# Optimization experiments

Hardware: AMD Instinct MI355X
Metric: run time of the kernel (lower is better)

## Reference

```python
import jax, jax.numpy as jnp
import numpy as np

NUM_EMBEDDINGS = 1024
EMBEDDING_DIM = 256
COMMITMENT_COST = 0.25


def setup_inputs() -> dict:
    key = jax.random.key(0)
    k1, k2 = jax.random.split(key)
    z = jax.random.normal(k1, (32, 256, 32, 32), dtype=jnp.float32)
    # matches torch init: uniform(-1/K, 1/K)
    codebook = jax.random.uniform(
        k2, (NUM_EMBEDDINGS, EMBEDDING_DIM), dtype=jnp.float32,
        minval=-1.0 / NUM_EMBEDDINGS, maxval=1.0 / NUM_EMBEDDINGS)
    return {"z": z, "codebook": codebook}


def reference(z, codebook):
    B, C, H, W = z.shape
    # b c h w -> (b h w) c
    z_nhwc = jnp.transpose(z, (0, 2, 3, 1))
    zf = z_nhwc.reshape(-1, C)  # [N, D]
    # squared euclidean distances [N, K]
    d = (jnp.sum(zf * zf, axis=1, keepdims=True)
         + jnp.sum(codebook * codebook, axis=1)
         - 2.0 * zf @ codebook.T)
    indices = jnp.argmin(d, axis=1)  # [N]
    zq_nhwc = codebook[indices].reshape(B, H, W, C)
    z_q = jnp.transpose(zq_nhwc, (0, 3, 1, 2))  # [B, C, H, W]

    codebook_loss = jnp.mean((jax.lax.stop_gradient(z_q) - z) ** 2)
    commitment_loss = jnp.mean((z_q - jax.lax.stop_gradient(z)) ** 2)
    vq_loss = codebook_loss + COMMITMENT_COST * commitment_loss

    # straight-through estimator
    z_q_st = z + jax.lax.stop_gradient(z_q - z)
    indices_bhw = indices.reshape(B, H, W)
    return z_q_st, vq_loss, indices_bhw
```

## Files before the change

kernel.cpp:

```cpp
#include <hip/hip_runtime.h>

#define NUM_EMB 1024
#define EMB_DIM 256
#define BATCH   32
#define HW      1024
#define Z_ELEMS (BATCH*EMB_DIM*HW)
#define LOSS_OFF Z_ELEMS
#define IDX_OFF (Z_ELEMS+1)

#define WS_CNORM_OFF 16
#define WS_ZNORM_OFF 2048
#define WS_PACKED_BYTE_OFF 262144
#define WS_NEEDED (WS_PACKED_BYTE_OFF + 32768*8)

typedef float v2f __attribute__((ext_vector_type(2)));

__global__ __launch_bounds__(256) void k_prep(const float* __restrict__ z,
                                              const float* __restrict__ cb,
                                              float* __restrict__ ws,
                                              unsigned long long* __restrict__ packed) {
    int gid = blockIdx.x * 256 + threadIdx.x;
    if (gid == 0) { ws[0] = 0.0f; ((unsigned int*)ws)[1] = 0u; }
    if (blockIdx.x < 4) {
        int k = gid;
        const float* row = cb + (size_t)k * EMB_DIM;
        float half[2];
#pragma unroll
        for (int h = 0; h < 2; ++h) {
            const float* a = row + h * 128;
            float r[8];
#pragma unroll
            for (int j = 0; j < 8; ++j) r[j] = __fmul_rn(a[j], a[j]);
            for (int i = 8; i < 128; i += 8)
#pragma unroll
                for (int j = 0; j < 8; ++j)
                    r[j] = __fadd_rn(r[j], __fmul_rn(a[i + j], a[i + j]));
            half[h] = __fadd_rn(__fadd_rn(__fadd_rn(r[0], r[1]), __fadd_rn(r[2], r[3])),
                                __fadd_rn(__fadd_rn(r[4], r[5]), __fadd_rn(r[6], r[7])));
        }
        ws[WS_CNORM_OFF + k] = __fadd_rn(half[0], half[1]);
    } else {
        int n = gid - 1024;
        packed[n] = 0xFFFFFFFFFFFFFFFFull;
        int b = n >> 10, p = n & 1023;
        const float* base = z + (size_t)b * EMB_DIM * HW + p;
        float half[2];
#pragma unroll
        for (int h = 0; h < 2; ++h) {
            float r[8];
#pragma unroll
            for (int j = 0; j < 8; ++j) {
                float v = base[(size_t)(h * 128 + j) * HW];
                r[j] = __fmul_rn(v, v);
            }
            for (int i = 8; i < 128; i += 8)
#pragma unroll
                for (int j = 0; j < 8; ++j) {
                    float v = base[(size_t)(h * 128 + i + j) * HW];
                    r[j] = __fadd_rn(r[j], __fmul_rn(v, v));
                }
            half[h] = __fadd_rn(__fadd_rn(__fadd_rn(r[0], r[1]), __fadd_rn(r[2], r[3])),
                                __fadd_rn(__fadd_rn(r[4], r[5]), __fadd_rn(r[6], r[7])));
        }
        ws[WS_ZNORM_OFF + n] = __fadd_rn(half[0], half[1]);
    }
}

#define MT 64
#define KC 256
#define DC 16
#define CPAD 260

__global__ __launch_bounds__(256, 4) void k_argmin(const float* __restrict__ z,
                                                   const float* __restrict__ cb,
                                                   const float* __restrict__ ws,
                                                   unsigned long long* __restrict__ packed) {
    __shared__ __attribute__((aligned(16))) float z_buf[DC * MT];
    __shared__ __attribute__((aligned(16))) float c_buf[DC * CPAD];

    const int tid = threadIdx.x;
    const int tx = tid & 15;
    const int ty = tid >> 4;
    const int b  = blockIdx.y;
    const int p0 = blockIdx.x * MT;
    const int kbase = blockIdx.z * 512;

    const float* zb = z + (size_t)b * EMB_DIM * HW + p0;
    const float* cn = ws + WS_CNORM_OFF;
    const float* zn = ws + WS_ZNORM_OFF + b * HW + p0;

    float z2[4];
#pragma unroll
    for (int a = 0; a < 4; ++a) z2[a] = zn[ty * 4 + a];

    float minv[4];
    int   mini[4];
#pragma unroll
    for (int a = 0; a < 4; ++a) { minv[a] = 3.402823466e+38f; mini[a] = 0; }

    const int zrow = tid >> 4;
    const int zcol = (tid & 15) << 2;

#pragma unroll 1
    for (int kc = 0; kc < 2; ++kc) {
        const int k0 = kbase + kc * KC;
        v2f acc2[4][8];
#pragma unroll
        for (int a = 0; a < 4; ++a)
#pragma unroll
            for (int j = 0; j < 8; ++j) acc2[a][j] = (v2f)(0.0f);

#pragma unroll 1
        for (int dc = 0; dc < EMB_DIM / DC; ++dc) {
            __syncthreads();
            {
                float4 v = *(const float4*)(zb + (size_t)(dc * DC + zrow) * HW + zcol);
                *(float4*)(z_buf + zrow * MT + zcol) = v;
            }
#pragma unroll
            for (int pass = 0; pass < 4; ++pass) {
                int idx = pass * 256 + tid;
                int kk  = idx >> 2;
                int seg = idx & 3;
                float4 v = *(const float4*)(cb + (size_t)(k0 + kk) * EMB_DIM + dc * DC + seg * 4);
                c_buf[(seg * 4 + 0) * CPAD + kk] = v.x;
                c_buf[(seg * 4 + 1) * CPAD + kk] = v.y;
                c_buf[(seg * 4 + 2) * CPAD + kk] = v.z;
                c_buf[(seg * 4 + 3) * CPAD + kk] = v.w;
            }
            __syncthreads();

#pragma unroll 2
            for (int d = 0; d < DC; ++d) {
                v2f za01 = *(const v2f*)(z_buf + d * MT + ty * 4);
                v2f za23 = *(const v2f*)(z_buf + d * MT + ty * 4 + 2);
                v2f cf2[8];
#pragma unroll
                for (int j = 0; j < 4; ++j) {
                    float4 cv = *(const float4*)(c_buf + d * CPAD + j * 64 + tx * 4);
                    cf2[j * 2 + 0] = (v2f){cv.x, cv.y};
                    cf2[j * 2 + 1] = (v2f){cv.z, cv.w};
                }
#pragma unroll
                for (int j = 0; j < 8; ++j) {
                    asm("v_pk_fma_f32 %0, %1, %2, %0 op_sel:[0,0,0] op_sel_hi:[0,1,1]"
                        : "+v"(acc2[0][j]) : "v"(za01), "v"(cf2[j]));
                    asm("v_pk_fma_f32 %0, %1, %2, %0 op_sel:[1,0,0] op_sel_hi:[1,1,1]"
                        : "+v"(acc2[1][j]) : "v"(za01), "v"(cf2[j]));
                    asm("v_pk_fma_f32 %0, %1, %2, %0 op_sel:[0,0,0] op_sel_hi:[0,1,1]"
                        : "+v"(acc2[2][j]) : "v"(za23), "v"(cf2[j]));
                    asm("v_pk_fma_f32 %0, %1, %2, %0 op_sel:[1,0,0] op_sel_hi:[1,1,1]"
                        : "+v"(acc2[3][j]) : "v"(za23), "v"(cf2[j]));
                }
            }
        }
        float c2[16];
#pragma unroll
        for (int j = 0; j < 4; ++j)
#pragma unroll
            for (int c = 0; c < 4; ++c)
                c2[j * 4 + c] = cn[k0 + j * 64 + tx * 4 + c];
#pragma unroll
        for (int a = 0; a < 4; ++a) {
#pragma unroll
            for (int j = 0; j < 4; ++j) {
#pragma unroll
                for (int c = 0; c < 4; ++c) {
                    int kg = k0 + j * 64 + tx * 4 + c;
                    float dot = acc2[a][j * 2 + (c >> 1)][c & 1];
                    float t1 = __fadd_rn(z2[a], c2[j * 4 + c]);
                    float s  = __fadd_rn(t1, __fmul_rn(-2.0f, dot));
                    if (s < minv[a]) { minv[a] = s; mini[a] = kg; }
                }
            }
        }
    }

    __syncthreads();
    float* rv = c_buf;
    int*   ri = (int*)(c_buf + 1024);
#pragma unroll
    for (int a = 0; a < 4; ++a) {
        int m = ty * 4 + a;
        rv[m * 16 + tx] = minv[a];
        ri[m * 16 + tx] = mini[a];
    }
    __syncthreads();
    if (tid < MT) {
        int m = tid;
        float bv = rv[m * 16];
        int   bi = ri[m * 16];
#pragma unroll
        for (int j = 1; j < 16; ++j) {
            float v  = rv[m * 16 + j];
            int   i2 = ri[m * 16 + j];
            if (v < bv || (v == bv && i2 < bi)) { bv = v; bi = i2; }
        }
        int n = b * HW + p0 + m;
        unsigned long long pk = ((unsigned long long)__float_as_uint(bv) << 32)
                                | (unsigned long long)(unsigned)bi;
        atomicMin(&packed[n], pk);
    }
}

__global__ __launch_bounds__(256) void k_merge(const unsigned long long* __restrict__ packed,
                                               float* __restrict__ out) {
    int n = blockIdx.x * 256 + threadIdx.x;
    out[IDX_OFF + n] = (float)(int)(unsigned)(packed[n] & 0xFFFFFFFFull);
}

__global__ __launch_bounds__(256) void k_gather(const float* __restrict__ z,
                                                const float* __restrict__ cb,
                                                float* __restrict__ out,
                                                float* __restrict__ ws,
                                                const unsigned long long* __restrict__ packed,
                                                int fused_idx) {
    __shared__ int   s_idx[64];
    __shared__ float s_red[4];
    const int tid = threadIdx.x;
    const int b  = blockIdx.x >> 4;
    const int p0 = (blockIdx.x & 15) * 64;

    if (tid < 64) {
        int n = b * HW + p0 + tid;
        int bi;
        if (fused_idx) {
            bi = (int)(unsigned)(packed[n] & 0xFFFFFFFFull);
            out[IDX_OFF + n] = (float)bi;
        } else {
            bi = (int)out[IDX_OFF + n];
        }
        s_idx[tid] = bi;
    }
    __syncthreads();

    const int p = tid & 63;
    const int cbase = tid >> 6;
    const int r = s_idx[p];
    const float* zrow = z   + (size_t)b * EMB_DIM * HW + p0 + p;
    float*       orow = out + (size_t)b * EMB_DIM * HW + p0 + p;
    const float* crow = cb  + (size_t)r * EMB_DIM;

    float acc = 0.0f;
#pragma unroll 4
    for (int it = 0; it < 64; ++it) {
        int c = it * 4 + cbase;
        float zq = crow[c];
        float zv = zrow[(size_t)c * HW];
        float d  = zq - zv;
        orow[(size_t)c * HW] = zv + d;
        acc += d * d;
    }
#pragma unroll
    for (int off = 32; off > 0; off >>= 1) acc += __shfl_down(acc, off, 64);
    if ((tid & 63) == 0) s_red[tid >> 6] = acc;
    __syncthreads();
    if (tid == 0) {
        atomicAdd(ws, s_red[0] + s_red[1] + s_red[2] + s_red[3]);
        __threadfence();
        unsigned old = atomicAdd((unsigned int*)ws + 1, 1u);
        if (old == 511u) {
            float total = atomicAdd(ws, 0.0f);
            out[LOSS_OFF] = 1.25f * (total * (1.0f / 8388608.0f));
        }
    }
}

extern "C" void kernel_launch(void* const* d_in, const int* in_sizes, int n_in,
                              void* d_out, int out_size, void* d_ws, size_t ws_size,
                              hipStream_t stream) {
    const float* z  = (const float*)d_in[0];
    const float* cb = (const float*)d_in[1];
    float* out = (float*)d_out;
    float* ws  = (float*)d_ws;

    const bool big_ws = (ws_size >= (size_t)WS_NEEDED);
    unsigned long long* packed = big_ws
        ? (unsigned long long*)((char*)d_ws + WS_PACKED_BYTE_OFF)
        : (unsigned long long*)d_out;

    k_prep  <<<132, 256, 0, stream>>>(z, cb, ws, packed);
    k_argmin<<<dim3(HW / MT, BATCH, 2), 256, 0, stream>>>(z, cb, ws, packed);
    if (!big_ws)
        k_merge<<<BATCH * HW / 256, 256, 0, stream>>>(packed, out);
    k_gather<<<BATCH * (HW / 64), 256, 0, stream>>>(z, cb, out, ws, packed, big_ws ? 1 : 0);
}
```

Before: 323.5 us.

## Prefetch argmin tiles into registers, split prep norms, stage gather codebook rows

The argmin kernel flattens its two loops into one 32-step loop. Each step loads the next z and codebook tile into registers while the current tile is written to LDS and computed, so global load latency is hidden behind the FMAs. The packed-FMA inline asm is replaced with scalar fmaf on a 4x16 accumulator, which may change register pressure and issue rate. The prep kernel now splits each z-norm across two threads and merges them through shared memory, doubling the number of blocks. The gather kernel stages codebook rows through a padded LDS tile for coalesced reads, at the cost of extra barriers.

Result: slower. 436.3 us (+34.9%).

```diff
diff --git a/kernel.cpp b/kernel.cpp
--- a/kernel.cpp
+++ b/kernel.cpp
@@ -13,16 +13,14 @@
 #define WS_PACKED_BYTE_OFF 262144
 #define WS_NEEDED (WS_PACKED_BYTE_OFF + 32768*8)
 
-typedef float v2f __attribute__((ext_vector_type(2)));
-
 __global__ __launch_bounds__(256) void k_prep(const float* __restrict__ z,
                                               const float* __restrict__ cb,
                                               float* __restrict__ ws,
                                               unsigned long long* __restrict__ packed) {
-    int gid = blockIdx.x * 256 + threadIdx.x;
-    if (gid == 0) { ws[0] = 0.0f; ((unsigned int*)ws)[1] = 0u; }
+    const int tid = threadIdx.x;
+    if (blockIdx.x == 0 && tid == 0) { ws[0] = 0.0f; ((unsigned int*)ws)[1] = 0u; }
     if (blockIdx.x < 4) {
-        int k = gid;
+        int k = blockIdx.x * 256 + tid;
         const float* row = cb + (size_t)k * EMB_DIM;
         float half[2];
 #pragma unroll
@@ -40,29 +38,31 @@
         }
         ws[WS_CNORM_OFF + k] = __fadd_rn(half[0], half[1]);
     } else {
-        int n = gid - 1024;
-        packed[n] = 0xFFFFFFFFFFFFFFFFull;
+        __shared__ float sh[256];
+        int n = (blockIdx.x - 4) * 128 + (tid >> 1);
+        int h = tid & 1;
         int b = n >> 10, p = n & 1023;
         const float* base = z + (size_t)b * EMB_DIM * HW + p;
-        float half[2];
-#pragma unroll
-        for (int h = 0; h < 2; ++h) {
-            float r[8];
+        float r[8];
+#pragma unroll
+        for (int j = 0; j < 8; ++j) {
+            float v = base[(size_t)(h * 128 + j) * HW];
+            r[j] = __fmul_rn(v, v);
+        }
+        for (int i = 8; i < 128; i += 8)
 #pragma unroll
             for (int j = 0; j < 8; ++j) {
-                float v = base[(size_t)(h * 128 + j) * HW];
-                r[j] = __fmul_rn(v, v);
+                float v = base[(size_t)(h * 128 + i + j) * HW];
+                r[j] = __fadd_rn(r[j], __fmul_rn(v, v));
             }
-            for (int i = 8; i < 128; i += 8)
-#pragma unroll
-                for (int j = 0; j < 8; ++j) {
-                    float v = base[(size_t)(h * 128 + i + j) * HW];
-                    r[j] = __fadd_rn(r[j], __fmul_rn(v, v));
-                }
-            half[h] = __fadd_rn(__fadd_rn(__fadd_rn(r[0], r[1]), __fadd_rn(r[2], r[3])),
-                                __fadd_rn(__fadd_rn(r[4], r[5]), __fadd_rn(r[6], r[7])));
-        }
-        ws[WS_ZNORM_OFF + n] = __fadd_rn(half[0], half[1]);
+        float half = __fadd_rn(__fadd_rn(__fadd_rn(r[0], r[1]), __fadd_rn(r[2], r[3])),
+                               __fadd_rn(__fadd_rn(r[4], r[5]), __fadd_rn(r[6], r[7])));
+        sh[tid] = half;
+        __syncthreads();
+        if (h == 0) {
+            ws[WS_ZNORM_OFF + n] = __fadd_rn(half, sh[tid + 1]);
+            packed[n] = 0xFFFFFFFFFFFFFFFFull;
+        }
     }
 }
 
@@ -100,79 +100,87 @@
 
     const int zrow = tid >> 4;
     const int zcol = (tid & 15) << 2;
+    const int ckk  = tid >> 2;
+    const int cseg = tid & 3;
+
+    float4 zpre = *(const float4*)(zb + (size_t)zrow * HW + zcol);
+    float4 cpre[4];
+#pragma unroll
+    for (int p = 0; p < 4; ++p)
+        cpre[p] = *(const float4*)(cb + (size_t)(kbase + p * 64 + ckk) * EMB_DIM + cseg * 4);
+
+    float acc[4][16];
+#pragma unroll
+    for (int a = 0; a < 4; ++a)
+#pragma unroll
+        for (int q = 0; q < 16; ++q) acc[a][q] = 0.0f;
 
 #pragma unroll 1
-    for (int kc = 0; kc < 2; ++kc) {
-        const int k0 = kbase + kc * KC;
-        v2f acc2[4][8];
-#pragma unroll
-        for (int a = 0; a < 4; ++a)
-#pragma unroll
-            for (int j = 0; j < 8; ++j) acc2[a][j] = (v2f)(0.0f);
-
-#pragma unroll 1
-        for (int dc = 0; dc < EMB_DIM / DC; ++dc) {
-            __syncthreads();
-            {
-                float4 v = *(const float4*)(zb + (size_t)(dc * DC + zrow) * HW + zcol);
-                *(float4*)(z_buf + zrow * MT + zcol) = v;
-            }
-#pragma unroll
-            for (int pass = 0; pass < 4; ++pass) {
-                int idx = pass * 256 + tid;
-                int kk  = idx >> 2;
-                int seg = idx & 3;
-                float4 v = *(const float4*)(cb + (size_t)(k0 + kk) * EMB_DIM + dc * DC + seg * 4);
-                c_buf[(seg * 4 + 0) * CPAD + kk] = v.x;
-                c_buf[(seg * 4 + 1) * CPAD + kk] = v.y;
-                c_buf[(seg * 4 + 2) * CPAD + kk] = v.z;
-                c_buf[(seg * 4 + 3) * CPAD + kk] = v.w;
-            }
-            __syncthreads();
-
-#pragma unroll 2
-            for (int d = 0; d < DC; ++d) {
-                v2f za01 = *(const v2f*)(z_buf + d * MT + ty * 4);
-                v2f za23 = *(const v2f*)(z_buf + d * MT + ty * 4 + 2);
-                v2f cf2[8];
-#pragma unroll
-                for (int j = 0; j < 4; ++j) {
-                    float4 cv = *(const float4*)(c_buf + d * CPAD + j * 64 + tx * 4);
-                    cf2[j * 2 + 0] = (v2f){cv.x, cv.y};
-                    cf2[j * 2 + 1] = (v2f){cv.z, cv.w};
-                }
-#pragma unroll
-                for (int j = 0; j < 8; ++j) {
-                    asm("v_pk_fma_f32 %0, %1, %2, %0 op_sel:[0,0,0] op_sel_hi:[0,1,1]"
-                        : "+v"(acc2[0][j]) : "v"(za01), "v"(cf2[j]));
-                    asm("v_pk_fma_f32 %0, %1, %2, %0 op_sel:[1,0,0] op_sel_hi:[1,1,1]"
-                        : "+v"(acc2[1][j]) : "v"(za01), "v"(cf2[j]));
-                    asm("v_pk_fma_f32 %0, %1, %2, %0 op_sel:[0,0,0] op_sel_hi:[0,1,1]"
-                        : "+v"(acc2[2][j]) : "v"(za23), "v"(cf2[j]));
-                    asm("v_pk_fma_f32 %0, %1, %2, %0 op_sel:[1,0,0] op_sel_hi:[1,1,1]"
-                        : "+v"(acc2[3][j]) : "v"(za23), "v"(cf2[j]));
+    for (int t = 0; t < 32; ++t) {
+        const int dc = t & 15;
+        const int kc = t >> 4;
+        __syncthreads();
+        *(float4*)(z_buf + zrow * MT + zcol) = zpre;
+#pragma unroll
+        for (int p = 0; p < 4; ++p) {
+            int kk = p * 64 + ckk;
+            c_buf[(cseg * 4 + 0) * CPAD + kk] = cpre[p].x;
+            c_buf[(cseg * 4 + 1) * CPAD + kk] = cpre[p].y;
+            c_buf[(cseg * 4 + 2) * CPAD + kk] = cpre[p].z;
+            c_buf[(cseg * 4 + 3) * CPAD + kk] = cpre[p].w;
+        }
+        if (t < 31) {
+            const int dc2 = (t + 1) & 15;
+            const int k02 = kbase + ((t + 1) >> 4) * KC;
+            zpre = *(const float4*)(zb + (size_t)(dc2 * DC + zrow) * HW + zcol);
+#pragma unroll
+            for (int p = 0; p < 4; ++p)
+                cpre[p] = *(const float4*)(cb + (size_t)(k02 + p * 64 + ckk) * EMB_DIM + dc2 * DC + cseg * 4);
+        }
+        __syncthreads();
+
+#pragma unroll 4
+        for (int d = 0; d < DC; ++d) {
+            float4 za = *(const float4*)(z_buf + d * MT + ty * 4);
+#pragma unroll
+            for (int j = 0; j < 4; ++j) {
+                float4 cv = *(const float4*)(c_buf + d * CPAD + j * 64 + tx * 4);
+#pragma unroll
+                for (int a = 0; a < 4; ++a) {
+                    float zf = (a == 0) ? za.x : (a == 1) ? za.y : (a == 2) ? za.z : za.w;
+                    acc[a][j * 4 + 0] = fmaf(zf, cv.x, acc[a][j * 4 + 0]);
+                    acc[a][j * 4 + 1] = fmaf(zf, cv.y, acc[a][j * 4 + 1]);
+                    acc[a][j * 4 + 2] = fmaf(zf, cv.z, acc[a][j * 4 + 2]);
+                    acc[a][j * 4 + 3] = fmaf(zf, cv.w, acc[a][j * 4 + 3]);
                 }
             }
         }
-        float c2[16];
-#pragma unroll
-        for (int j = 0; j < 4; ++j)
-#pragma unroll
-            for (int c = 0; c < 4; ++c)
-                c2[j * 4 + c] = cn[k0 + j * 64 + tx * 4 + c];
-#pragma unroll
-        for (int a = 0; a < 4; ++a) {
-#pragma unroll
-            for (int j = 0; j < 4; ++j) {
-#pragma unroll
-                for (int c = 0; c < 4; ++c) {
-                    int kg = k0 + j * 64 + tx * 4 + c;
-                    float dot = acc2[a][j * 2 + (c >> 1)][c & 1];
-                    float t1 = __fadd_rn(z2[a], c2[j * 4 + c]);
-                    float s  = __fadd_rn(t1, __fmul_rn(-2.0f, dot));
-                    if (s < minv[a]) { minv[a] = s; mini[a] = kg; }
+
+        if (dc == 15) {
+            const int k0 = kbase + kc * KC;
+            float c2[16];
+#pragma unroll
+            for (int j = 0; j < 4; ++j)
+#pragma unroll
+                for (int c = 0; c < 4; ++c)
+                    c2[j * 4 + c] = cn[k0 + j * 64 + tx * 4 + c];
+#pragma unroll
+            for (int a = 0; a < 4; ++a) {
+#pragma unroll
+                for (int j = 0; j < 4; ++j) {
+#pragma unroll
+                    for (int c = 0; c < 4; ++c) {
+                        int kg = k0 + j * 64 + tx * 4 + c;
+                        float t1 = __fadd_rn(z2[a], c2[j * 4 + c]);
+                        float s  = __fadd_rn(t1, __fmul_rn(-2.0f, acc[a][j * 4 + c]));
+                        if (s < minv[a]) { minv[a] = s; mini[a] = kg; }
+                    }
                 }
             }
+#pragma unroll
+            for (int a = 0; a < 4; ++a)
+#pragma unroll
+                for (int q = 0; q < 16; ++q) acc[a][q] = 0.0f;
         }
     }
 
@@ -215,6 +223,7 @@
                                                 float* __restrict__ ws,
                                                 const unsigned long long* __restrict__ packed,
                                                 int fused_idx) {
+    __shared__ float s_cb[64][65];
     __shared__ int   s_idx[64];
     __shared__ float s_red[4];
     const int tid = threadIdx.x;
@@ -234,22 +243,33 @@
     }
     __syncthreads();
 
-    const int p = tid & 63;
-    const int cbase = tid >> 6;
-    const int r = s_idx[p];
+    const int p    = tid & 63;
+    const int cgrp = tid >> 6;
+    const int row  = tid >> 2;
+    const int q4   = tid & 3;
     const float* zrow = z   + (size_t)b * EMB_DIM * HW + p0 + p;
     float*       orow = out + (size_t)b * EMB_DIM * HW + p0 + p;
-    const float* crow = cb  + (size_t)r * EMB_DIM;
 
     float acc = 0.0f;
-#pragma unroll 4
-    for (int it = 0; it < 64; ++it) {
-        int c = it * 4 + cbase;
-        float zq = crow[c];
-        float zv = zrow[(size_t)c * HW];
-        float d  = zq - zv;
-        orow[(size_t)c * HW] = zv + d;
-        acc += d * d;
+#pragma unroll 1
+    for (int d0 = 0; d0 < EMB_DIM; d0 += 64) {
+        const float* cr = cb + (size_t)s_idx[row] * EMB_DIM + d0;
+#pragma unroll
+        for (int pass = 0; pass < 4; ++pass) {
+            int c = q4 * 4 + pass * 16;
+            *(float4*)(&s_cb[row][c]) = *(const float4*)(cr + c);
+        }
+        __syncthreads();
+#pragma unroll
+        for (int j = 0; j < 16; ++j) {
+            int c = cgrp * 16 + j;
+            float zq = s_cb[p][c];
+            float zv = zrow[(size_t)(d0 + c) * HW];
+            float d  = zq - zv;
+            orow[(size_t)(d0 + c) * HW] = zv + d;
+            acc += d * d;
+        }
+        __syncthreads();
     }
 #pragma unroll
     for (int off = 32; off > 0; off >>= 1) acc += __shfl_down(acc, off, 64);
@@ -279,7 +299,7 @@
         ? (unsigned long long*)((char*)d_ws + WS_PACKED_BYTE_OFF)
         : (unsigned long long*)d_out;
 
-    k_prep  <<<132, 256, 0, stream>>>(z, cb, ws, packed);
+    k_prep  <<<260, 256, 0, stream>>>(z, cb, ws, packed);
     k_argmin<<<dim3(HW / MT, BATCH, 2), 256, 0, stream>>>(z, cb, ws, packed);
     if (!big_ws)
         k_merge<<<BATCH * HW / 256, 256, 0, stream>>>(packed, out);
```
